# Kernel tuning notes

Measured on AMD Instinct MI355X. Metric: run time of the kernel, lower is better.

The kernel has to match this reference:

```python
import jax, jax.numpy as jnp
import numpy as np

DIM = 1024
HEADS = 16
EPS = 1e-05
B, T, C, H, W = 2, 16, DIM, 32, 32


def setup_inputs() -> dict:
    key = jax.random.key(0)
    ks = jax.random.split(key, 4)
    s = 1.0 / np.sqrt(DIM)
    return {
        "x": jax.random.normal(ks[0], (B, T, C, H, W), dtype=jnp.float32),
        "ln_w": jnp.ones((C,), dtype=jnp.float32),
        "ln_b": jnp.zeros((C,), dtype=jnp.float32),
        "Wq": jax.random.normal(ks[1], (C, C), dtype=jnp.float32) * s,
        "Wk": jax.random.normal(ks[2], (C, C), dtype=jnp.float32) * s,
        "Wv": jax.random.normal(ks[3], (C, C), dtype=jnp.float32) * s,
    }


def reference(x, ln_w, ln_b, Wq, Wk, Wv):
    b, t, c, h, w = x.shape
    heads = HEADS
    dh = c // heads
    scale = dh ** (-0.5)

    # Channel LayerNorm: normalize over C per (b,t,h,w)
    xc = jnp.transpose(x, (0, 1, 3, 4, 2))  # [B,T,H,W,C]
    mu = jnp.mean(xc, axis=-1, keepdims=True)
    var = jnp.mean(jnp.square(xc - mu), axis=-1, keepdims=True)
    xn = (xc - mu) * jax.lax.rsqrt(var + EPS) * ln_w + ln_b  # [B,T,H,W,C]

    # Q/K from spatial mean-pool
    pooled = jnp.mean(xn, axis=(2, 3))  # [B,T,C]
    q = pooled @ Wq.T  # [B,T,C]
    k = pooled @ Wk.T  # [B,T,C]

    # V per pixel; torch permutes to [B,W,H,T,C] then flattens W-major
    v = jnp.transpose(xn, (0, 3, 2, 1, 4)).reshape(b, h * w, t, c)  # [B,HW(w-major),T,C]
    v = v @ Wv.T

    q = q.reshape(b, t, heads, dh).transpose(0, 2, 1, 3) * scale  # [B,h,T,dh]
    k = k.reshape(b, t, heads, dh).transpose(0, 2, 3, 1)          # [B,h,dh,T]
    v = v.reshape(b, h * w, t, heads, dh).transpose(0, 1, 3, 2, 4)  # [B,HW,h,T,dh]

    attn = jax.nn.softmax(jnp.matmul(q, k), axis=-1)  # [B,h,T,T]
    out = jnp.einsum('bhst,bnhtd->bnhsd', attn, v)    # [B,HW,h,T,dh]
    # permute(0,3,2,4,1) -> [B,T,h,dh,HW], then view as (H,W)
    out = out.transpose(0, 3, 2, 4, 1).reshape(b, t, c, h, w)
    return out
```

## Files before the change

kernel.cpp:

```cpp
#include <hip/hip_runtime.h>
#include <stdint.h>
#include <stddef.h>

#define CDIM 1024
#define HWD  1024
#define TD   16
#define BD   2
#define NH   16
#define DHD  64

typedef __attribute__((ext_vector_type(8))) short bf16x8;
typedef __attribute__((ext_vector_type(4))) short bf16x4;
typedef __attribute__((ext_vector_type(4))) float f32x4;

static __device__ __forceinline__ short f2bf(float f) {
  uint32_t u = __builtin_bit_cast(uint32_t, f);
  uint32_t r = (u + 0x7FFFu + ((u >> 16) & 1u)) >> 16;
  return (short)(uint16_t)r;
}
static __device__ __forceinline__ float bf2f(short s) {
  return __builtin_bit_cast(float, (uint32_t)((uint16_t)s) << 16);
}

static __device__ __forceinline__ void gl_lds16(const short* g, short* l) {
  __builtin_amdgcn_global_load_lds((const __attribute__((address_space(1))) unsigned int*)g,
                                   (__attribute__((address_space(3))) unsigned int*)l,
                                   16, 0, 0);
}

__global__ void k_cast3(const float* __restrict__ Wq, const float* __restrict__ Wk,
                        const float* __restrict__ Wv, short* __restrict__ Wqkb,
                        short* __restrict__ Wb) {
  int bid = blockIdx.x;
  int mat = bid >> 10;
  const float* src = mat == 0 ? Wq : (mat == 1 ? Wk : Wv);
  short* dst = mat == 0 ? Wqkb : (mat == 1 ? Wqkb + 1048576 : Wb);
  int i = ((bid & 1023) * 256 + threadIdx.x) * 4;
  f32x4 v = *(const f32x4*)&src[i];
  dst[i + 0] = f2bf(v[0]);
  dst[i + 1] = f2bf(v[1]);
  dst[i + 2] = f2bf(v[2]);
  dst[i + 3] = f2bf(v[3]);
}

__global__ __launch_bounds__(1024) void k_ln_stats(const float* __restrict__ x,
                                                   float* __restrict__ partials) {
  int bt = blockIdx.y;
  int c0 = blockIdx.x * 32;
  int tid = threadIdx.x;
  int quad = tid & 255, rowoff = tid >> 8;
  const float* xs = x + (size_t)bt * CDIM * HWD;

  float s[4] = {}, s2[4] = {};
  #pragma unroll
  for (int j = 0; j < 8; ++j) {
    int c = c0 + rowoff + 4 * j;
    f32x4 v = *(const f32x4*)&xs[(size_t)c * HWD + quad * 4];
    #pragma unroll
    for (int i = 0; i < 4; ++i) { s[i] += v[i]; s2[i] += v[i] * v[i]; }
  }
  __shared__ float redA[4][1024], redB[4][1024];
  #pragma unroll
  for (int i = 0; i < 4; ++i) {
    redA[rowoff][quad * 4 + i] = s[i];
    redB[rowoff][quad * 4 + i] = s2[i];
  }
  __syncthreads();
  int px = tid;
  float a  = redA[0][px] + redA[1][px] + redA[2][px] + redA[3][px];
  float b2 = redB[0][px] + redB[1][px] + redB[2][px] + redB[3][px];
  float* pb = partials + ((size_t)(bt * 32 + blockIdx.x) * 2) * HWD;
  pb[px] = a;
  pb[HWD + px] = b2;
}

__global__ void k_ln_fin(const float* __restrict__ partials, float* __restrict__ stats) {
  int bt = blockIdx.y;
  int px = blockIdx.x * 256 + threadIdx.x;
  float a = 0.f, b2 = 0.f;
  #pragma unroll
  for (int sp = 0; sp < 32; ++sp) {
    const float* pb = partials + ((size_t)(bt * 32 + sp) * 2) * HWD;
    a += pb[px];
    b2 += pb[HWD + px];
  }
  float mu = a * (1.0f / CDIM);
  float var = b2 * (1.0f / CDIM) - mu * mu;
  stats[(size_t)bt * 2 * HWD + px] = mu;
  stats[(size_t)bt * 2 * HWD + HWD + px] = rsqrtf(var + 1e-5f);
}

__global__ __launch_bounds__(256) void k_ln_norm(const float* __restrict__ x,
                                                 const float* __restrict__ lnw,
                                                 const float* __restrict__ lnb,
                                                 const float* __restrict__ stats,
                                                 short* __restrict__ xnT,
                                                 float* __restrict__ part) {
  int bt = blockIdx.y;
  int pg = blockIdx.x;
  int P0 = pg * 32;
  int tid = threadIdx.x;
  int pq = tid & 7, rowgrp = tid >> 3;
  const float* xs = x + (size_t)bt * CDIM * HWD;
  short* outB = xnT + (size_t)bt * CDIM * HWD;

  f32x4 mu4 = *(const f32x4*)&stats[(size_t)bt * 2 * HWD + P0 + pq * 4];
  f32x4 rs4 = *(const f32x4*)&stats[(size_t)bt * 2 * HWD + HWD + P0 + pq * 4];

  __shared__ short tile[32 * 514];
  __shared__ float prA[512][8];

  for (int ch = 0; ch < 2; ++ch) {
    #pragma unroll
    for (int j = 0; j < 16; ++j) {
      int cl = rowgrp + 32 * j;
      int c = ch * 512 + cl;
      f32x4 v = *(const f32x4*)&xs[(size_t)c * HWD + P0 + pq * 4];
      float w = lnw[c], bb = lnb[c];
      int cc = cl >> 3, c7 = cl & 7;
      float psum = 0.f;
      #pragma unroll
      for (int i = 0; i < 4; ++i) {
        int px = pq * 4 + i;
        float xn = (v[i] - mu4[i]) * rs4[i] * w + bb;
        psum += xn;
        tile[px * 514 + ((cc ^ (px & 7)) << 3) + c7] = f2bf(xn);
      }
      prA[cl][pq] = psum;
    }
    __syncthreads();
    {
      int qr = tid & 31, seg = tid >> 5;
      int q = qr * 32 + pg;
      short* dst = outB + (size_t)q * CDIM + ch * 512 + seg * 64;
      #pragma unroll
      for (int mm = 0; mm < 8; ++mm) {
        int cc = seg * 8 + mm;
        bf16x8 vv = *(const bf16x8*)&tile[qr * 514 + ((cc ^ (qr & 7)) << 3)];
        *(bf16x8*)&dst[mm * 8] = vv;
      }
    }
    #pragma unroll
    for (int rep = 0; rep < 2; ++rep) {
      int cl = rep * 256 + tid;
      float a = 0.f;
      #pragma unroll
      for (int k = 0; k < 8; ++k) a += prA[cl][k];
      part[((size_t)(bt * 32 + pg)) * CDIM + ch * 512 + cl] = a;
    }
    __syncthreads();
  }
}

__global__ void k_pool_red(const float* __restrict__ part, short* __restrict__ pooledb) {
  int bt = blockIdx.y;
  int c = blockIdx.x * 256 + threadIdx.x;
  float s = 0.f;
  #pragma unroll
  for (int pc = 0; pc < 32; ++pc) s += part[((size_t)(bt * 32 + pc)) * CDIM + c];
  pooledb[bt * CDIM + c] = f2bf(s * (1.0f / HWD));
}

__global__ __launch_bounds__(256) void k_qk_mfma(const short* __restrict__ Wqkb,
                                                 const short* __restrict__ pooledb,
                                                 float* __restrict__ qm,
                                                 float* __restrict__ km) {
  int n0 = blockIdx.x * 128;
  __shared__ __align__(16) short lA[32 * 32];
  __shared__ __align__(16) short lB[128 * 32];
  int tid = threadIdx.x, lane = tid & 63, wid = tid >> 6;
  int s0 = wid * 128 + lane, s1 = s0 + 64;
  int fr = lane & 15, fk = (lane >> 4) * 8;
  f32x4 acc[2][2] = {};

  for (int kt = 0; kt < CDIM / 32; ++kt) {
    int k0 = kt * 32;
    __syncthreads();
    gl_lds16(&Wqkb[(size_t)(n0 + (s0 >> 2)) * CDIM + k0 + (s0 & 3) * 8], &lB[s0 * 8]);
    gl_lds16(&Wqkb[(size_t)(n0 + (s1 >> 2)) * CDIM + k0 + (s1 & 3) * 8], &lB[s1 * 8]);
    if (wid < 2) {
      gl_lds16(&pooledb[(size_t)(tid >> 2) * CDIM + k0 + (tid & 3) * 8], &lA[tid * 8]);
    }
    __syncthreads();
    bf16x8 af[2], bfr[2];
    #pragma unroll
    for (int mi = 0; mi < 2; ++mi)
      af[mi] = *(const bf16x8*)&lA[(mi * 16 + fr) * 32 + fk];
    #pragma unroll
    for (int ni = 0; ni < 2; ++ni)
      bfr[ni] = *(const bf16x8*)&lB[(wid * 32 + ni * 16 + fr) * 32 + fk];
    #pragma unroll
    for (int mi = 0; mi < 2; ++mi)
      #pragma unroll
      for (int ni = 0; ni < 2; ++ni)
        acc[mi][ni] = __builtin_amdgcn_mfma_f32_16x16x32_bf16(af[mi], bfr[ni], acc[mi][ni], 0, 0, 0);
  }

  int cr = lane >> 4;
  #pragma unroll
  for (int mi = 0; mi < 2; ++mi)
    #pragma unroll
    for (int ni = 0; ni < 2; ++ni)
      #pragma unroll
      for (int rr = 0; rr < 4; ++rr) {
        int row = mi * 16 + cr * 4 + rr;
        int col = n0 + wid * 32 + ni * 16 + fr;
        float v = acc[mi][ni][rr];
        if (col < 1024) qm[(size_t)row * CDIM + col] = v;
        else            km[(size_t)row * CDIM + col - 1024] = v;
      }
}

__global__ void k_attn(const float* __restrict__ qm, const float* __restrict__ km,
                       float* __restrict__ attn) {
  int bg = blockIdx.x;
  int b = bg >> 4, g = bg & 15;
  int s = threadIdx.x >> 4, t = threadIdx.x & 15;
  const float* qr = qm + (size_t)(b * TD + s) * CDIM + g * DHD;
  const float* kr = km + (size_t)(b * TD + t) * CDIM + g * DHD;
  float d = 0.f;
  #pragma unroll
  for (int i = 0; i < DHD; ++i) d += qr[i] * kr[i];
  d *= 0.125f;
  float m = d;
  #pragma unroll
  for (int off = 8; off; off >>= 1) m = fmaxf(m, __shfl_xor(m, off, 16));
  float e = __expf(d - m);
  float sum = e;
  #pragma unroll
  for (int off = 8; off; off >>= 1) sum += __shfl_xor(sum, off, 16);
  attn[(size_t)bg * 256 + s * 16 + t] = e / sum;
}

__global__ __launch_bounds__(512, 2) void k_vgemm(const short* __restrict__ Wb,
                                                  const short* __restrict__ xnT,
                                                  short* __restrict__ vp) {
  int bid = blockIdx.x;
  int swz = (bid & 7) * 64 + (bid >> 3);
  int bt = swz >> 4;
  int m0 = ((swz >> 2) & 3) * 256;
  int n0 = (swz & 3) * 256;
  const short* Bm = xnT + (size_t)bt * CDIM * HWD;

  __shared__ __align__(16) short lA[2][256 * 64];
  __shared__ __align__(16) short lB[2][256 * 64];

  int tid = threadIdx.x, lane = tid & 63, wid = tid >> 6;
  int wm = wid >> 2, wn = wid & 3;

  int srow = wid * 8 + (lane >> 3);
  int schunk = (lane & 7) ^ (lane >> 3);
  const short* gA = Wb + (size_t)(m0 + srow) * CDIM + schunk * 8;
  const short* gB = Bm + (size_t)(n0 + srow) * CDIM + schunk * 8;
  int doff = wid * 512 + lane * 8;

  int fr = lane & 15, klane = lane >> 4;
  int c0 = ((klane ^ (fr & 7)) * 8);
  int rA = (wm * 128 + fr) * 64;
  int rB = (wn * 64 + fr) * 64;

  f32x4 acc[8][4] = {};
  bf16x8 bq[4], af[4];

#define ISSUE(p, kt1, nb)                                                      \
  do {                                                                         \
    gl_lds16(gA + (size_t)(p) * 64 * CDIM + (kt1) * 64, &lA[nb][(p) * 4096 + doff]); \
    gl_lds16(gB + (size_t)(p) * 64 * CDIM + (kt1) * 64, &lB[nb][(p) * 4096 + doff]); \
  } while (0)
#define RDA(mi, ks, b) (*(const bf16x8*)&lA[b][rA + (mi) * 1024 + (c0 ^ ((ks) * 32))])
#define RDB(ni, ks, b) (*(const bf16x8*)&lB[b][rB + (ni) * 1024 + (c0 ^ ((ks) * 32))])

  ISSUE(0, 0, 0); ISSUE(1, 0, 0); ISSUE(2, 0, 0); ISSUE(3, 0, 0);

  for (int kt = 0; kt < 16; ++kt) {
    int cur = kt & 1, nxt = cur ^ 1;
    bool st = (kt + 1 < 16);
    if (st) {
      ISSUE(0, kt + 1, nxt);
      asm volatile("s_waitcnt vmcnt(2)" ::: "memory");
    } else {
      asm volatile("s_waitcnt vmcnt(0)" ::: "memory");
    }
    __builtin_amdgcn_s_barrier();
    #pragma unroll
    for (int ni = 0; ni < 4; ++ni) bq[ni] = RDB(ni, 0, cur);
    #pragma unroll
    for (int mi = 0; mi < 4; ++mi) af[mi] = RDA(mi, 0, cur);
    __builtin_amdgcn_s_setprio(1);
    #pragma unroll
    for (int mi = 0; mi < 4; ++mi)
      #pragma unroll
      for (int ni = 0; ni < 4; ++ni)
        acc[mi][ni] = __builtin_amdgcn_mfma_f32_16x16x32_bf16(af[mi], bq[ni], acc[mi][ni], 0, 0, 0);
    __builtin_amdgcn_s_setprio(0);
    __builtin_amdgcn_s_barrier();
    #pragma unroll
    for (int mi = 0; mi < 4; ++mi) af[mi] = RDA(4 + mi, 0, cur);
    if (st) ISSUE(1, kt + 1, nxt);
    __builtin_amdgcn_s_barrier();
    __builtin_amdgcn_s_setprio(1);
    #pragma unroll
    for (int mi = 0; mi < 4; ++mi)
      #pragma unroll
      for (int ni = 0; ni < 4; ++ni)
        acc[4 + mi][ni] = __builtin_amdgcn_mfma_f32_16x16x32_bf16(af[mi], bq[ni], acc[4 + mi][ni], 0, 0, 0);
    __builtin_amdgcn_s_setprio(0);
    __builtin_amdgcn_s_barrier();
    #pragma unroll
    for (int ni = 0; ni < 4; ++ni) bq[ni] = RDB(ni, 1, cur);
    #pragma unroll
    for (int mi = 0; mi < 4; ++mi) af[mi] = RDA(mi, 1, cur);
    if (st) ISSUE(2, kt + 1, nxt);
    __builtin_amdgcn_s_barrier();
    __builtin_amdgcn_s_setprio(1);
    #pragma unroll
    for (int mi = 0; mi < 4; ++mi)
      #pragma unroll
      for (int ni = 0; ni < 4; ++ni)
        acc[mi][ni] = __builtin_amdgcn_mfma_f32_16x16x32_bf16(af[mi], bq[ni], acc[mi][ni], 0, 0, 0);
    __builtin_amdgcn_s_setprio(0);
    __builtin_amdgcn_s_barrier();
    #pragma unroll
    for (int mi = 0; mi < 4; ++mi) af[mi] = RDA(4 + mi, 1, cur);
    if (st) ISSUE(3, kt + 1, nxt);
    __builtin_amdgcn_s_barrier();
    __builtin_amdgcn_s_setprio(1);
    #pragma unroll
    for (int mi = 0; mi < 4; ++mi)
      #pragma unroll
      for (int ni = 0; ni < 4; ++ni)
        acc[4 + mi][ni] = __builtin_amdgcn_mfma_f32_16x16x32_bf16(af[mi], bq[ni], acc[4 + mi][ni], 0, 0, 0);
    __builtin_amdgcn_s_setprio(0);
    __builtin_amdgcn_s_barrier();
  }
#undef ISSUE
#undef RDA
#undef RDB

  short* outB = vp + (size_t)bt * CDIM * HWD;
  int cr = lane >> 4;
  #pragma unroll
  for (int mi = 0; mi < 8; ++mi)
    #pragma unroll
    for (int ni = 0; ni < 4; ++ni)
      #pragma unroll
      for (int r = 0; r < 4; ++r) {
        int row = m0 + wm * 128 + mi * 16 + cr * 4 + r;
        int col = n0 + wn * 64 + ni * 16 + fr;
        outB[(size_t)row * HWD + col] = f2bf(acc[mi][ni][r]);
      }
}

__global__ __launch_bounds__(256) void k_mix(const short* __restrict__ vp,
                                             const float* __restrict__ attn,
                                             float* __restrict__ out) {
  int c = blockIdx.x;
  int b = blockIdx.y;
  int g = c >> 6;
  __shared__ __align__(16) short vpl[TD * HWD];
  __shared__ float at[256];
  int tid = threadIdx.x;
  at[tid] = attn[(size_t)(b * NH + g) * 256 + tid];
  #pragma unroll
  for (int j = 0; j < 8; ++j) {
    int chunk = j * 256 + tid;
    int t = chunk >> 7, qc = chunk & 127;
    bf16x8 v = *(const bf16x8*)&vp[((size_t)(b * TD + t) * CDIM + c) * HWD + qc * 8];
    *(bf16x8*)&vpl[t * HWD + qc * 8] = v;
  }
  __syncthreads();
  int p = tid * 4;
  #pragma unroll
  for (int sh = 0; sh < 2; ++sh) {
    f32x4 acc[8] = {};
    #pragma unroll
    for (int t = 0; t < TD; ++t) {
      bf16x4 v4 = *(const bf16x4*)&vpl[t * HWD + p];
      f32x4 vf = {bf2f(v4[0]), bf2f(v4[1]), bf2f(v4[2]), bf2f(v4[3])};
      #pragma unroll
      for (int s8 = 0; s8 < 8; ++s8) {
        float a = at[(sh * 8 + s8) * 16 + t];
        acc[s8] += a * vf;
      }
    }
    #pragma unroll
    for (int s8 = 0; s8 < 8; ++s8) {
      int s = sh * 8 + s8;
      *(f32x4*)&out[((size_t)(b * TD + s) * CDIM + c) * HWD + p] = acc[s8];
    }
  }
}

extern "C" void kernel_launch(void* const* d_in, const int* in_sizes, int n_in,
                              void* d_out, int out_size, void* d_ws, size_t ws_size,
                              hipStream_t stream) {
  const float* x   = (const float*)d_in[0];
  const float* lnw = (const float*)d_in[1];
  const float* lnb = (const float*)d_in[2];
  const float* Wq  = (const float*)d_in[3];
  const float* Wk  = (const float*)d_in[4];
  const float* Wv  = (const float*)d_in[5];
  float* out = (float*)d_out;

  char* ws = (char*)d_ws;
  const size_t XNT_OFF   = 0;
  const size_t VP_OFF    = XNT_OFF + 67108864;
  const size_t WB_OFF    = VP_OFF + 67108864;
  const size_t WQKB_OFF  = WB_OFF + 2097152;
  const size_t POOLB_OFF = WQKB_OFF + 4194304;
  const size_t QM_OFF    = POOLB_OFF + 65536;
  const size_t KM_OFF    = QM_OFF + 131072;
  const size_t ATTN_OFF  = KM_OFF + 131072;

  short* xnT    = (short*)(ws + XNT_OFF);
  short* vp     = (short*)(ws + VP_OFF);
  float* partials = (float*)(ws + VP_OFF);
  float* part     = (float*)(ws + VP_OFF + 8388608);
  float* stats    = (float*)(ws + VP_OFF + 8388608 + 4194304);
  short* Wb     = (short*)(ws + WB_OFF);
  short* Wqkb   = (short*)(ws + WQKB_OFF);
  short* poolb  = (short*)(ws + POOLB_OFF);
  float* qm     = (float*)(ws + QM_OFF);
  float* km     = (float*)(ws + KM_OFF);
  float* attn   = (float*)(ws + ATTN_OFF);

  k_cast3<<<dim3(3072), 256, 0, stream>>>(Wq, Wk, Wv, Wqkb, Wb);
  k_ln_stats<<<dim3(32, 32), 1024, 0, stream>>>(x, partials);
  k_ln_fin<<<dim3(4, 32), 256, 0, stream>>>(partials, stats);
  k_ln_norm<<<dim3(32, 32), 256, 0, stream>>>(x, lnw, lnb, stats, xnT, part);
  k_pool_red<<<dim3(4, 32), 256, 0, stream>>>(part, poolb);
  k_qk_mfma<<<dim3(16), 256, 0, stream>>>(Wqkb, poolb, qm, km);
  k_attn<<<dim3(32), 256, 0, stream>>>(qm, km, attn);
  k_vgemm<<<dim3(512), 512, 0, stream>>>(Wb, xnT, vp);
  k_mix<<<dim3(1024, 2), 256, 0, stream>>>(vp, attn, out);
}
```

Measured before the change: 239.2 us.

## Fuse LayerNorm stats, finalize and normalize into one register-resident kernel

```diff
diff --git a/kernel.cpp b/kernel.cpp
--- a/kernel.cpp
+++ b/kernel.cpp
@@ -43,86 +43,67 @@
   dst[i + 3] = f2bf(v[3]);
 }
 
-__global__ __launch_bounds__(1024) void k_ln_stats(const float* __restrict__ x,
-                                                   float* __restrict__ partials) {
-  int bt = blockIdx.y;
-  int c0 = blockIdx.x * 32;
-  int tid = threadIdx.x;
-  int quad = tid & 255, rowoff = tid >> 8;
-  const float* xs = x + (size_t)bt * CDIM * HWD;
-
-  float s[4] = {}, s2[4] = {};
-  #pragma unroll
-  for (int j = 0; j < 8; ++j) {
-    int c = c0 + rowoff + 4 * j;
-    f32x4 v = *(const f32x4*)&xs[(size_t)c * HWD + quad * 4];
-    #pragma unroll
-    for (int i = 0; i < 4; ++i) { s[i] += v[i]; s2[i] += v[i] * v[i]; }
-  }
-  __shared__ float redA[4][1024], redB[4][1024];
-  #pragma unroll
-  for (int i = 0; i < 4; ++i) {
-    redA[rowoff][quad * 4 + i] = s[i];
-    redB[rowoff][quad * 4 + i] = s2[i];
-  }
-  __syncthreads();
-  int px = tid;
-  float a  = redA[0][px] + redA[1][px] + redA[2][px] + redA[3][px];
-  float b2 = redB[0][px] + redB[1][px] + redB[2][px] + redB[3][px];
-  float* pb = partials + ((size_t)(bt * 32 + blockIdx.x) * 2) * HWD;
-  pb[px] = a;
-  pb[HWD + px] = b2;
-}
-
-__global__ void k_ln_fin(const float* __restrict__ partials, float* __restrict__ stats) {
-  int bt = blockIdx.y;
-  int px = blockIdx.x * 256 + threadIdx.x;
-  float a = 0.f, b2 = 0.f;
-  #pragma unroll
-  for (int sp = 0; sp < 32; ++sp) {
-    const float* pb = partials + ((size_t)(bt * 32 + sp) * 2) * HWD;
-    a += pb[px];
-    b2 += pb[HWD + px];
-  }
-  float mu = a * (1.0f / CDIM);
-  float var = b2 * (1.0f / CDIM) - mu * mu;
-  stats[(size_t)bt * 2 * HWD + px] = mu;
-  stats[(size_t)bt * 2 * HWD + HWD + px] = rsqrtf(var + 1e-5f);
-}
-
-__global__ __launch_bounds__(256) void k_ln_norm(const float* __restrict__ x,
-                                                 const float* __restrict__ lnw,
-                                                 const float* __restrict__ lnb,
-                                                 const float* __restrict__ stats,
-                                                 short* __restrict__ xnT,
-                                                 float* __restrict__ part) {
+__global__ __launch_bounds__(256) void k_ln(const float* __restrict__ x,
+                                            const float* __restrict__ lnw,
+                                            const float* __restrict__ lnb,
+                                            short* __restrict__ xnT,
+                                            float* __restrict__ part) {
   int bt = blockIdx.y;
   int pg = blockIdx.x;
   int P0 = pg * 32;
   int tid = threadIdx.x;
-  int pq = tid & 7, rowgrp = tid >> 3;
+  int pq = tid & 7, cr = tid >> 3;
   const float* xs = x + (size_t)bt * CDIM * HWD;
   short* outB = xnT + (size_t)bt * CDIM * HWD;
 
-  f32x4 mu4 = *(const f32x4*)&stats[(size_t)bt * 2 * HWD + P0 + pq * 4];
-  f32x4 rs4 = *(const f32x4*)&stats[(size_t)bt * 2 * HWD + HWD + P0 + pq * 4];
+  f32x4 v[32];
+  float s[4] = {}, s2[4] = {};
+  #pragma unroll
+  for (int j = 0; j < 32; ++j) {
+    int c = cr + 32 * j;
+    v[j] = *(const f32x4*)&xs[(size_t)c * HWD + P0 + pq * 4];
+    #pragma unroll
+    for (int i = 0; i < 4; ++i) { s[i] += v[j][i]; s2[i] += v[j][i] * v[j][i]; }
+  }
+  __shared__ float redA[32][33], redB[32][33];
+  #pragma unroll
+  for (int i = 0; i < 4; ++i) {
+    redA[cr][pq * 4 + i] = s[i];
+    redB[cr][pq * 4 + i] = s2[i];
+  }
+  __syncthreads();
+  __shared__ float muS[32], rsS[32];
+  if (tid < 32) {
+    float a = 0.f, b2 = 0.f;
+    #pragma unroll
+    for (int k = 0; k < 32; ++k) { a += redA[k][tid]; b2 += redB[k][tid]; }
+    float mu = a * (1.0f / CDIM);
+    float var = b2 * (1.0f / CDIM) - mu * mu;
+    muS[tid] = mu;
+    rsS[tid] = rsqrtf(var + 1e-5f);
+  }
+  __syncthreads();
+  float mu_[4], rs_[4];
+  #pragma unroll
+  for (int i = 0; i < 4; ++i) { mu_[i] = muS[pq * 4 + i]; rs_[i] = rsS[pq * 4 + i]; }
 
   __shared__ short tile[32 * 514];
   __shared__ float prA[512][8];
 
+  #pragma unroll
   for (int ch = 0; ch < 2; ++ch) {
     #pragma unroll
-    for (int j = 0; j < 16; ++j) {
-      int cl = rowgrp + 32 * j;
+    for (int jj = 0; jj < 16; ++jj) {
+      int j = ch * 16 + jj;
+      int cl = cr + 32 * jj;
       int c = ch * 512 + cl;
-      f32x4 v = *(const f32x4*)&xs[(size_t)c * HWD + P0 + pq * 4];
       float w = lnw[c], bb = lnb[c];
       int cc = cl >> 3, c7 = cl & 7;
       float psum = 0.f;
       #pragma unroll
       for (int i = 0; i < 4; ++i) {
         int px = pq * 4 + i;
-        float xn = (v[i] - mu4[i]) * rs4[i] * w + bb;
+        float xn = (v[j][i] - mu_[i]) * rs_[i] * w + bb;
         psum += xn;
         tile[px * 514 + ((cc ^ (px & 7)) << 3) + c7] = f2bf(xn);
       }
@@ -414,9 +395,7 @@
 
   short* xnT    = (short*)(ws + XNT_OFF);
   short* vp     = (short*)(ws + VP_OFF);
-  float* partials = (float*)(ws + VP_OFF);
-  float* part     = (float*)(ws + VP_OFF + 8388608);
-  float* stats    = (float*)(ws + VP_OFF + 8388608 + 4194304);
+  float* part   = (float*)(ws + VP_OFF);
   short* Wb     = (short*)(ws + WB_OFF);
   short* Wqkb   = (short*)(ws + WQKB_OFF);
   short* poolb  = (short*)(ws + POOLB_OFF);
@@ -425,9 +404,7 @@
   float* attn   = (float*)(ws + ATTN_OFF);
 
   k_cast3<<<dim3(3072), 256, 0, stream>>>(Wq, Wk, Wv, Wqkb, Wb);
-  k_ln_stats<<<dim3(32, 32), 1024, 0, stream>>>(x, partials);
-  k_ln_fin<<<dim3(4, 32), 256, 0, stream>>>(partials, stats);
-  k_ln_norm<<<dim3(32, 32), 256, 0, stream>>>(x, lnw, lnb, stats, xnT, part);
+  k_ln<<<dim3(32, 32), 256, 0, stream>>>(x, lnw, lnb, xnT, part);
   k_pool_red<<<dim3(4, 32), 256, 0, stream>>>(part, poolb);
   k_qk_mfma<<<dim3(16), 256, 0, stream>>>(Wqkb, poolb, qm, km);
   k_attn<<<dim3(32), 256, 0, stream>>>(qm, km, attn);
```

New measurement: 195.4 us. 18.3% less time.
